# Performance work log

Measured on AMD Instinct MI355X. Metric: run time of the kernel, lower is better.

Reference implementation:

```python
import jax, jax.numpy as jnp
import numpy as np

N_NODES = 20000
N_EDGES = 320000
D_IN = 128
D_HID = 128
D_OUT = 128
HEADS = 4
NEG_SLOPE = 0.2
BN_EPS = 1e-5


def _gat_conv(x, src, dst, W, a_src, a_dst, b):
    """PyG GATConv with concat=False (mean over heads). Self-loops already in src/dst."""
    N = x.shape[0]
    H, C = a_src.shape
    h = (x @ W).reshape(N, H, C)                     # [N,H,C] per-head projections
    alpha_s = jnp.sum(h * a_src, axis=-1)            # [N,H]
    alpha_d = jnp.sum(h * a_dst, axis=-1)            # [N,H]
    logits = jax.nn.leaky_relu(alpha_s[src] + alpha_d[dst], NEG_SLOPE)  # [E,H]
    # segment softmax over incoming edges of each destination node
    m = jax.ops.segment_max(logits, dst, num_segments=N)               # [N,H]
    e = jnp.exp(logits - m[dst])
    z = jax.ops.segment_sum(e, dst, num_segments=N)                     # [N,H]
    alpha = e / (z[dst] + 1e-16)                                        # [E,H]
    msg = h[src] * alpha[:, :, None]                                    # [E,H,C]
    out = jax.ops.segment_sum(msg, dst, num_segments=N)                 # [N,H,C]
    return jnp.mean(out, axis=1) + b                                    # [N,C]


def _bn(x, gamma, beta):
    mu = jnp.mean(x, axis=0)
    var = jnp.var(x, axis=0)
    return (x - mu) * jax.lax.rsqrt(var + BN_EPS) * gamma + beta


def setup_inputs() -> dict:
    key = jax.random.key(0)
    ks = jax.random.split(key, 24)
    inp = {
        'x': jax.random.normal(ks[0], (N_NODES, D_IN), jnp.float32),
        'edge_index': jax.random.randint(ks[1], (2, N_EDGES), 0, N_NODES, jnp.int64),
        'edge_attr': jax.random.normal(ks[2], (N_EDGES, 16), jnp.float32),
    }
    def glorot(k, shape):
        fan = sum(shape) if len(shape) > 1 else shape[0]
        return jax.random.normal(k, shape, jnp.float32) * np.float32(np.sqrt(2.0 / fan))
    dims = [(D_IN, D_HID), (D_HID, D_HID), (D_HID, D_OUT)]
    for i, (din, dout) in enumerate(dims):
        inp[f'W{i}'] = glorot(ks[3 + 4 * i], (din, HEADS * dout))
        inp[f'asrc{i}'] = glorot(ks[4 + 4 * i], (HEADS, dout))
        inp[f'adst{i}'] = glorot(ks[5 + 4 * i], (HEADS, dout))
        inp[f'b{i}'] = jnp.zeros((dout,), jnp.float32)
    for i in range(2):
        inp[f'gamma{i}'] = jnp.ones((D_HID,), jnp.float32)
        inp[f'beta{i}'] = jnp.zeros((D_HID,), jnp.float32)
    return inp


def reference(x, edge_index, edge_attr, W0, asrc0, adst0, b0, gamma0, beta0,
              W1, asrc1, adst1, b1, gamma1, beta1, W2, asrc2, adst2, b2):
    N = x.shape[0]
    ar = jnp.arange(N, dtype=edge_index.dtype)
    src = jnp.concatenate([edge_index[0], ar])  # add self-loops (PyG default)
    dst = jnp.concatenate([edge_index[1], ar])
    h = _gat_conv(x, src, dst, W0, asrc0, adst0, b0)
    h = jax.nn.relu(_bn(h, gamma0, beta0))
    h = _gat_conv(h, src, dst, W1, asrc1, adst1, b1)
    h = jax.nn.relu(_bn(h, gamma1, beta1))
    out = _gat_conv(h, src, dst, W2, asrc2, adst2, b2)
    return (out, edge_attr)
```

## Files before the change

kernel.cpp:

```cpp
#include <hip/hip_runtime.h>
#include <hip/hip_fp16.h>
#include <math.h>

#define N_NODES 20000
#define N_EDGES 320000
#define EN (N_EDGES + N_NODES)
#define DIM 128
#define HEADS 4
#define DH (HEADS * DIM)
#define NEG_SLOPE 0.2f
#define BN_EPS 1e-5f

typedef _Float16 h4 __attribute__((ext_vector_type(4)));
typedef _Float16 h8 __attribute__((ext_vector_type(8)));
typedef float f4 __attribute__((ext_vector_type(4)));

__device__ __forceinline__ float lrelu(float x) { return x > 0.f ? x : NEG_SLOPE * x; }


__global__ __launch_bounds__(256) void build_edges_kernel(
    const void* __restrict__ ei_raw, int* __restrict__ src32,
    int* __restrict__ dst32, int* __restrict__ deg) {
  int e = blockIdx.x * 256 + threadIdx.x;
  if (e >= EN) return;
  const long long* ei64 = (const long long*)ei_raw;
  const int* ei32 = (const int*)ei_raw;
  bool is64 = true;
#pragma unroll
  for (int k = 0; k < 4; ++k) {
    long long v = ei64[k];
    if (v < 0 || v >= N_NODES) is64 = false;
  }
  int s, d;
  if (e < N_EDGES) {
    if (is64) { s = (int)ei64[e]; d = (int)ei64[N_EDGES + e]; }
    else      { s = ei32[e];      d = ei32[N_EDGES + e]; }
  } else {
    s = d = e - N_EDGES;
  }
  src32[e] = s;
  dst32[e] = d;
  atomicAdd(&deg[d], 1);
}

__global__ __launch_bounds__(1024) void scan_kernel(
    const int* __restrict__ deg, int* __restrict__ off) {
  __shared__ int sums[1024];
  const int tid = threadIdx.x;
  const int chunk = (N_NODES + 1023) / 1024;
  int start = tid * chunk;
  int end = start + chunk; if (end > N_NODES) end = N_NODES;
  int s = 0;
  for (int i = start; i < end && i < N_NODES; ++i) s += deg[i];
  sums[tid] = s;
  __syncthreads();
  for (int st = 1; st < 1024; st <<= 1) {
    int t = (tid >= st) ? sums[tid - st] : 0;
    __syncthreads();
    sums[tid] += t;
    __syncthreads();
  }
  int run = sums[tid] - s;
  for (int i = start; i < end && i < N_NODES; ++i) { off[i] = run; run += deg[i]; }
  if (tid == 1023) off[N_NODES] = sums[1023];
}

__global__ __launch_bounds__(256) void scatter_kernel(
    const int* __restrict__ src32, const int* __restrict__ dst32,
    const int* __restrict__ off, int* __restrict__ cursor,
    int* __restrict__ csrc) {
  int e = blockIdx.x * 256 + threadIdx.x;
  if (e >= EN) return;
  int d = dst32[e];
  int pos = atomicAdd(&cursor[d], 1);
  csrc[off[d] + pos] = src32[e];
}


__global__ __launch_bounds__(128) void wtrans_kernel(
    const float* __restrict__ W, __half* __restrict__ Wt) {
  int n = blockIdx.x;
  int k = threadIdx.x;
  Wt[(size_t)n * 128 + k] = __float2half(W[(size_t)k * 512 + n]);
}


#define SWZ(r, byte_in_row) (((r) * 256 + (byte_in_row)) ^ (((r) & 7) << 4))

__global__ __launch_bounds__(256) void gemm_mfma_kernel(
    const float* __restrict__ A, const __half* __restrict__ Wt,
    ushort* __restrict__ H16, int M) {
  __shared__ __align__(16) char Xt[64 * 256];
  __shared__ __align__(16) char Wl[64 * 256];
  int tid = threadIdx.x;
  int brow = blockIdx.x * 64;
  int bn = blockIdx.y * 64;
#pragma unroll
  for (int it = 0; it < 8; ++it) {
    int idx = it * 256 + tid;
    int r = idx >> 5, c4 = idx & 31;
    int row = brow + r;
    float4 v = make_float4(0.f, 0.f, 0.f, 0.f);
    if (row < M) v = *(const float4*)&A[(size_t)row * 128 + c4 * 4];
    h4 hv;
    hv[0] = (_Float16)v.x; hv[1] = (_Float16)v.y;
    hv[2] = (_Float16)v.z; hv[3] = (_Float16)v.w;
    *(h4*)(Xt + SWZ(r, c4 * 8)) = hv;
  }
#pragma unroll
  for (int it = 0; it < 4; ++it) {
    int idx = it * 256 + tid;
    int r = idx >> 4, c4 = idx & 15;
    uint4 v = *(const uint4*)&Wt[(size_t)(bn + r) * 128 + c4 * 8];
    *(uint4*)(Wl + SWZ(r, c4 * 16)) = v;
  }
  __syncthreads();
  int wave = tid >> 6, lane = tid & 63;
  int lrow = lane & 15, kgrp = lane >> 4;
  f4 acc[4] = {};
#pragma unroll
  for (int ks = 0; ks < 4; ++ks) {
    int kb = ks * 64 + kgrp * 16;
    int wr = wave * 16 + lrow;
    h8 af = *(h8*)(Wl + SWZ(wr, kb));
#pragma unroll
    for (int mt = 0; mt < 4; ++mt) {
      int xr = mt * 16 + lrow;
      h8 bf = *(h8*)(Xt + SWZ(xr, kb));
      acc[mt] = __builtin_amdgcn_mfma_f32_16x16x32_f16(af, bf, acc[mt], 0, 0, 0);
    }
  }
#pragma unroll
  for (int mt = 0; mt < 4; ++mt) {
    int m = brow + mt * 16 + lrow;
    if (m < M) {
      h4 hv;
#pragma unroll
      for (int i = 0; i < 4; ++i) hv[i] = (_Float16)acc[mt][i];
      *(h4*)&H16[(size_t)m * DH + bn + wave * 16 + kgrp * 4] = hv;
    }
  }
}


__global__ __launch_bounds__(256) void alpha_kernel(
    const ushort* __restrict__ H16, const float* __restrict__ a_src,
    const float* __restrict__ a_dst, float* __restrict__ as_,
    float* __restrict__ ad_) {
  int n = blockIdx.x;
  int head = threadIdx.x >> 6;
  int lane = threadIdx.x & 63;
  const __half2* hp = (const __half2*)(H16 + (size_t)n * DH) + head * 64 + lane;
  float2 h = __half22float2(*hp);
  float s = h.x * a_src[head * DIM + 2 * lane] + h.y * a_src[head * DIM + 2 * lane + 1];
  float d = h.x * a_dst[head * DIM + 2 * lane] + h.y * a_dst[head * DIM + 2 * lane + 1];
#pragma unroll
  for (int o = 32; o > 0; o >>= 1) {
    s += __shfl_xor(s, o);
    d += __shfl_xor(d, o);
  }
  if (lane == 0) {
    as_[n * 4 + head] = s;
    ad_[n * 4 + head] = d;
  }
}


__global__ __launch_bounds__(256) void smagg_kernel(
    const ushort* __restrict__ H16, const float* __restrict__ as_,
    const float* __restrict__ ad_, const int* __restrict__ off,
    const int* __restrict__ csrc, const float* __restrict__ bias,
    float* __restrict__ out, float* __restrict__ galpha) {
  __shared__ float4 alds[2][64];
  __shared__ float4 xred[2][32];
  int tid = threadIdx.x;
  int half = tid >> 7;
  int n = blockIdx.x * 2 + half;
  int wv = (tid >> 6) & 1;
  int lane = tid & 63;
  int e0 = off[n], e1 = off[n + 1];
  int deg = e1 - e0;
  bool fast = (deg <= 64);
  if (wv == 0) {
    float4 ad = *(const float4*)&ad_[n * 4];
    if (fast) {
      int i = e0 + lane;
      bool valid = lane < deg;
      float l0 = -1e30f, l1 = -1e30f, l2 = -1e30f, l3 = -1e30f;
      if (valid) {
        int s = csrc[i];
        float4 av = *(const float4*)&as_[s * 4];
        l0 = lrelu(av.x + ad.x); l1 = lrelu(av.y + ad.y);
        l2 = lrelu(av.z + ad.z); l3 = lrelu(av.w + ad.w);
      }
      float m0 = l0, m1 = l1, m2 = l2, m3 = l3;
#pragma unroll
      for (int o = 32; o > 0; o >>= 1) {
        m0 = fmaxf(m0, __shfl_xor(m0, o)); m1 = fmaxf(m1, __shfl_xor(m1, o));
        m2 = fmaxf(m2, __shfl_xor(m2, o)); m3 = fmaxf(m3, __shfl_xor(m3, o));
      }
      float p0 = valid ? expf(l0 - m0) : 0.f;
      float p1 = valid ? expf(l1 - m1) : 0.f;
      float p2 = valid ? expf(l2 - m2) : 0.f;
      float p3 = valid ? expf(l3 - m3) : 0.f;
      float z0 = p0, z1 = p1, z2 = p2, z3 = p3;
#pragma unroll
      for (int o = 32; o > 0; o >>= 1) {
        z0 += __shfl_xor(z0, o); z1 += __shfl_xor(z1, o);
        z2 += __shfl_xor(z2, o); z3 += __shfl_xor(z3, o);
      }
      if (valid) {
        alds[half][lane] = make_float4(p0 / (z0 + 1e-16f), p1 / (z1 + 1e-16f),
                                       p2 / (z2 + 1e-16f), p3 / (z3 + 1e-16f));
      }
    } else {
      float m0 = -1e30f, m1 = -1e30f, m2 = -1e30f, m3 = -1e30f;
      for (int i = e0 + lane; i < e1; i += 64) {
        int s = csrc[i];
        float4 av = *(const float4*)&as_[s * 4];
        float l0 = lrelu(av.x + ad.x), l1 = lrelu(av.y + ad.y);
        float l2 = lrelu(av.z + ad.z), l3 = lrelu(av.w + ad.w);
        ((float4*)galpha)[i] = make_float4(l0, l1, l2, l3);
        m0 = fmaxf(m0, l0); m1 = fmaxf(m1, l1);
        m2 = fmaxf(m2, l2); m3 = fmaxf(m3, l3);
      }
#pragma unroll
      for (int o = 32; o > 0; o >>= 1) {
        m0 = fmaxf(m0, __shfl_xor(m0, o)); m1 = fmaxf(m1, __shfl_xor(m1, o));
        m2 = fmaxf(m2, __shfl_xor(m2, o)); m3 = fmaxf(m3, __shfl_xor(m3, o));
      }
      float z0 = 0.f, z1 = 0.f, z2 = 0.f, z3 = 0.f;
      for (int i = e0 + lane; i < e1; i += 64) {
        float4 l = ((const float4*)galpha)[i];
        float p0 = expf(l.x - m0), p1 = expf(l.y - m1);
        float p2 = expf(l.z - m2), p3 = expf(l.w - m3);
        ((float4*)galpha)[i] = make_float4(p0, p1, p2, p3);
        z0 += p0; z1 += p1; z2 += p2; z3 += p3;
      }
#pragma unroll
      for (int o = 32; o > 0; o >>= 1) {
        z0 += __shfl_xor(z0, o); z1 += __shfl_xor(z1, o);
        z2 += __shfl_xor(z2, o); z3 += __shfl_xor(z3, o);
      }
      float r0 = 1.f / (z0 + 1e-16f), r1 = 1.f / (z1 + 1e-16f);
      float r2 = 1.f / (z2 + 1e-16f), r3 = 1.f / (z3 + 1e-16f);
      for (int i = e0 + lane; i < e1; i += 64) {
        float4 p = ((const float4*)galpha)[i];
        ((float4*)galpha)[i] = make_float4(p.x * r0, p.y * r1, p.z * r2, p.w * r3);
      }
    }
  }
  __syncthreads();
  const uint2* Hp = (const uint2*)H16;
  const float* alds_f = (const float*)&alds[half][0];
  int hh = wv * 2 + (lane >> 5);
  float a0 = 0.f, a1 = 0.f, a2 = 0.f, a3 = 0.f;
  int i = e0;
#define AGG_BODY(ii)                                                          \
  {                                                                           \
    int s = csrc[ii];                                                         \
    float w = fast ? alds_f[((ii) - e0) * 4 + hh] : galpha[(size_t)(ii) * 4 + hh]; \
    uint2 hvv = Hp[(size_t)s * 128 + wv * 64 + lane];                         \
    float2 lo = __half22float2(*(__half2*)&hvv.x);                            \
    float2 hi = __half22float2(*(__half2*)&hvv.y);                            \
    a0 += w * lo.x; a1 += w * lo.y; a2 += w * hi.x; a3 += w * hi.y;           \
  }
  for (; i + 3 < e1; i += 4) { AGG_BODY(i) AGG_BODY(i + 1) AGG_BODY(i + 2) AGG_BODY(i + 3) }
  for (; i < e1; ++i) AGG_BODY(i)
#undef AGG_BODY
  a0 += __shfl_xor(a0, 32); a1 += __shfl_xor(a1, 32);
  a2 += __shfl_xor(a2, 32); a3 += __shfl_xor(a3, 32);
  if (wv == 1 && lane < 32) xred[half][lane] = make_float4(a0, a1, a2, a3);
  __syncthreads();
  if (wv == 0 && lane < 32) {
    float4 o2 = xred[half][lane];
    float4 bv = *(const float4*)&bias[lane * 4];
    float4 r;
    r.x = 0.25f * (a0 + o2.x) + bv.x;
    r.y = 0.25f * (a1 + o2.y) + bv.y;
    r.z = 0.25f * (a2 + o2.z) + bv.z;
    r.w = 0.25f * (a3 + o2.w) + bv.w;
    *(float4*)&out[(size_t)n * DIM + lane * 4] = r;
  }
}


__global__ __launch_bounds__(256) void bn_stats_kernel(
    const float* __restrict__ X, float* __restrict__ stats) {
  int c = threadIdx.x & 127;
  int half = threadIdx.x >> 7;
  float s = 0.f, s2 = 0.f;
  for (int r = blockIdx.x * 2 + half; r < N_NODES; r += gridDim.x * 2) {
    float v = X[(size_t)r * DIM + c];
    s += v;
    s2 += v * v;
  }
  atomicAdd(&stats[c], s);
  atomicAdd(&stats[DIM + c], s2);
}

__global__ __launch_bounds__(256) void bn_apply_kernel(
    float* __restrict__ X, const float* __restrict__ stats,
    const float* __restrict__ gamma, const float* __restrict__ beta) {
  int idx = blockIdx.x * 256 + threadIdx.x;
  if (idx >= N_NODES * DIM) return;
  int c = idx & 127;
  const float invN = 1.f / (float)N_NODES;
  float mean = stats[c] * invN;
  float var = stats[DIM + c] * invN - mean * mean;
  float scale = gamma[c] * rsqrtf(var + BN_EPS);
  float shift = beta[c] - mean * scale;
  float v = X[idx] * scale + shift;
  X[idx] = fmaxf(v, 0.f);
}


extern "C" void kernel_launch(void* const* d_in, const int* in_sizes, int n_in,
                              void* d_out, int out_size, void* d_ws, size_t ws_size,
                              hipStream_t stream) {
  (void)in_sizes; (void)n_in; (void)out_size; (void)ws_size;
  const float* x = (const float*)d_in[0];
  const void* ei = d_in[1];
  const float* eattr = (const float*)d_in[2];
  const float* W[3]    = {(const float*)d_in[3],  (const float*)d_in[7],  (const float*)d_in[11]};
  const float* asrc[3] = {(const float*)d_in[4],  (const float*)d_in[8],  (const float*)d_in[12]};
  const float* adst[3] = {(const float*)d_in[5],  (const float*)d_in[9],  (const float*)d_in[13]};
  const float* bias[3] = {(const float*)d_in[6],  (const float*)d_in[10], (const float*)d_in[14]};
  const float* gamma[2] = {(const float*)d_in[15], (const float*)d_in[17]};
  const float* beta[2]  = {(const float*)d_in[16], (const float*)d_in[18]};

  char* ws = (char*)d_ws;
  size_t o = 0;
  auto alloc = [&](size_t bytes) -> void* {
    void* p = ws + o;
    o += (bytes + 255) & ~(size_t)255;
    return p;
  };
  int* deg      = (int*)alloc(N_NODES * 4);
  int* cursor   = (int*)alloc(N_NODES * 4);
  float* stats0 = (float*)alloc(2 * DIM * 4);
  float* stats1 = (float*)alloc(2 * DIM * 4);
  size_t zero_bytes = o;
  int* off    = (int*)alloc((N_NODES + 1) * 4);
  int* src32  = (int*)alloc((size_t)EN * 4);
  int* dst32  = (int*)alloc((size_t)EN * 4);
  int* csrc   = (int*)alloc((size_t)EN * 4);
  float* galpha = (float*)alloc((size_t)EN * 4 * 4);
  ushort* H16  = (ushort*)alloc((size_t)N_NODES * DH * 2);
  float* Ob    = (float*)alloc((size_t)N_NODES * DIM * 4);
  float* as_   = (float*)alloc((size_t)N_NODES * 4 * 4);
  float* ad_   = (float*)alloc((size_t)N_NODES * 4 * 4);
  __half* Wt[3];
  for (int L = 0; L < 3; ++L) Wt[L] = (__half*)alloc((size_t)DH * 128 * 2);

  hipMemsetAsync(d_ws, 0, zero_bytes, stream);

  build_edges_kernel<<<(EN + 255) / 256, 256, 0, stream>>>(ei, src32, dst32, deg);
  scan_kernel<<<1, 1024, 0, stream>>>(deg, off);
  scatter_kernel<<<(EN + 255) / 256, 256, 0, stream>>>(src32, dst32, off, cursor, csrc);
  for (int L = 0; L < 3; ++L)
    wtrans_kernel<<<DH, 128, 0, stream>>>(W[L], Wt[L]);

  const float* in_ptr = x;
  for (int L = 0; L < 3; ++L) {
    gemm_mfma_kernel<<<dim3((N_NODES + 63) / 64, DH / 64), 256, 0, stream>>>(
        in_ptr, Wt[L], H16, N_NODES);
    alpha_kernel<<<N_NODES, 256, 0, stream>>>(H16, asrc[L], adst[L], as_, ad_);
    float* outp = (L == 2) ? (float*)d_out : Ob;
    smagg_kernel<<<N_NODES / 2, 256, 0, stream>>>(H16, as_, ad_, off, csrc,
                                                  bias[L], outp, galpha);
    if (L < 2) {
      float* st = (L == 0) ? stats0 : stats1;
      bn_stats_kernel<<<256, 256, 0, stream>>>(Ob, st);
      bn_apply_kernel<<<(N_NODES * DIM + 255) / 256, 256, 0, stream>>>(
          Ob, st, gamma[L], beta[L]);
      in_ptr = Ob;
    }
  }

  hipMemcpyAsync((float*)d_out + (size_t)N_NODES * DIM, eattr,
                 (size_t)N_EDGES * 16 * 4, hipMemcpyDeviceToDevice, stream);
}
```

Measured before the change: 536.4 us.

## Fuse alpha and BN-apply into GEMM, widen aggregation to one wave per node

The GEMM kernel now computes the per-head attention dot products from its accumulators, which removes the separate alpha kernel and its re-read of H16. It also applies the BatchNorm scale/shift and ReLU while loading its input, so a small coefficient kernel replaces the full bn_apply pass. The aggregation kernel maps one wave per node with 16-byte gathers and an 8-way unroll, dropping the LDS cross-wave reduction and __syncthreads. The three weight transposes are merged into one launch. Each GEMM block now loops over four N-chunks, which cuts the grid width and adds serial work per block.

```diff
diff --git a/kernel.cpp b/kernel.cpp
--- a/kernel.cpp
+++ b/kernel.cpp
@@ -78,90 +78,143 @@
 
 
 __global__ __launch_bounds__(128) void wtrans_kernel(
-    const float* __restrict__ W, __half* __restrict__ Wt) {
+    const float* __restrict__ W0, const float* __restrict__ W1,
+    const float* __restrict__ W2, __half* __restrict__ T0,
+    __half* __restrict__ T1, __half* __restrict__ T2) {
   int n = blockIdx.x;
   int k = threadIdx.x;
-  Wt[(size_t)n * 128 + k] = __float2half(W[(size_t)k * 512 + n]);
+  const float* W = (blockIdx.y == 0) ? W0 : (blockIdx.y == 1) ? W1 : W2;
+  __half* T = (blockIdx.y == 0) ? T0 : (blockIdx.y == 1) ? T1 : T2;
+  T[(size_t)n * 128 + k] = __float2half(W[(size_t)k * 512 + n]);
+}
+
+
+__global__ __launch_bounds__(128) void bn_coef_kernel(
+    const float* __restrict__ stats, const float* __restrict__ gamma,
+    const float* __restrict__ beta, float* __restrict__ coef) {
+  int c = threadIdx.x;
+  const float invN = 1.f / (float)N_NODES;
+  float mean = stats[c] * invN;
+  float var = stats[DIM + c] * invN - mean * mean;
+  float scale = gamma[c] * rsqrtf(var + BN_EPS);
+  coef[c] = scale;
+  coef[DIM + c] = beta[c] - mean * scale;
 }
 
 
 #define SWZ(r, byte_in_row) (((r) * 256 + (byte_in_row)) ^ (((r) & 7) << 4))
 
-__global__ __launch_bounds__(256) void gemm_mfma_kernel(
+__global__ __launch_bounds__(256) void gemm_fused_kernel(
     const float* __restrict__ A, const __half* __restrict__ Wt,
-    ushort* __restrict__ H16, int M) {
+    const float* __restrict__ coef, int apply_bn,
+    const float* __restrict__ a_src, const float* __restrict__ a_dst,
+    ushort* __restrict__ H16, float* __restrict__ as_,
+    float* __restrict__ ad_, int M) {
   __shared__ __align__(16) char Xt[64 * 256];
   __shared__ __align__(16) char Wl[64 * 256];
+  __shared__ float red_as[4][4][2][16];
+  __shared__ float red_ad[4][4][2][16];
   int tid = threadIdx.x;
   int brow = blockIdx.x * 64;
-  int bn = blockIdx.y * 64;
+  int half_id = blockIdx.y;
+  const float4* coef4 = (const float4*)coef;
 #pragma unroll
   for (int it = 0; it < 8; ++it) {
     int idx = it * 256 + tid;
     int r = idx >> 5, c4 = idx & 31;
     int row = brow + r;
     float4 v = make_float4(0.f, 0.f, 0.f, 0.f);
-    if (row < M) v = *(const float4*)&A[(size_t)row * 128 + c4 * 4];
+    if (row < M) {
+      v = *(const float4*)&A[(size_t)row * 128 + c4 * 4];
+      if (apply_bn) {
+        float4 sc = coef4[c4], sh = coef4[32 + c4];
+        v.x = fmaxf(v.x * sc.x + sh.x, 0.f);
+        v.y = fmaxf(v.y * sc.y + sh.y, 0.f);
+        v.z = fmaxf(v.z * sc.z + sh.z, 0.f);
+        v.w = fmaxf(v.w * sc.w + sh.w, 0.f);
+      }
+    }
     h4 hv;
     hv[0] = (_Float16)v.x; hv[1] = (_Float16)v.y;
     hv[2] = (_Float16)v.z; hv[3] = (_Float16)v.w;
     *(h4*)(Xt + SWZ(r, c4 * 8)) = hv;
   }
-#pragma unroll
-  for (int it = 0; it < 4; ++it) {
-    int idx = it * 256 + tid;
-    int r = idx >> 4, c4 = idx & 15;
-    uint4 v = *(const uint4*)&Wt[(size_t)(bn + r) * 128 + c4 * 8];
-    *(uint4*)(Wl + SWZ(r, c4 * 16)) = v;
-  }
-  __syncthreads();
   int wave = tid >> 6, lane = tid & 63;
   int lrow = lane & 15, kgrp = lane >> 4;
-  f4 acc[4] = {};
-#pragma unroll
-  for (int ks = 0; ks < 4; ++ks) {
-    int kb = ks * 64 + kgrp * 16;
-    int wr = wave * 16 + lrow;
-    h8 af = *(h8*)(Wl + SWZ(wr, kb));
+  float asum[4][2] = {}, adsum[4][2] = {};
+  for (int nc = 0; nc < 4; ++nc) {
+    int chunk = half_id * 4 + nc;
+    int hh = nc >> 1;
+    __syncthreads();
+#pragma unroll
+    for (int it = 0; it < 4; ++it) {
+      int idx = it * 256 + tid;
+      int r = idx >> 4, c4 = idx & 15;
+      uint4 v = *(const uint4*)&Wt[(size_t)(chunk * 64 + r) * 128 + c4 * 8];
+      *(uint4*)(Wl + SWZ(r, c4 * 16)) = v;
+    }
+    __syncthreads();
+    f4 acc[4] = {};
+#pragma unroll
+    for (int ks = 0; ks < 4; ++ks) {
+      int kb = ks * 64 + kgrp * 16;
+      h8 af = *(h8*)(Wl + SWZ(wave * 16 + lrow, kb));
+#pragma unroll
+      for (int mt = 0; mt < 4; ++mt) {
+        h8 bf = *(h8*)(Xt + SWZ(mt * 16 + lrow, kb));
+        acc[mt] = __builtin_amdgcn_mfma_f32_16x16x32_f16(af, bf, acc[mt], 0, 0, 0);
+      }
+    }
+    int n_base = chunk * 64 + wave * 16 + kgrp * 4;
+    float4 as4 = *(const float4*)&a_src[n_base];
+    float4 ad4 = *(const float4*)&a_dst[n_base];
 #pragma unroll
     for (int mt = 0; mt < 4; ++mt) {
-      int xr = mt * 16 + lrow;
-      h8 bf = *(h8*)(Xt + SWZ(xr, kb));
-      acc[mt] = __builtin_amdgcn_mfma_f32_16x16x32_f16(af, bf, acc[mt], 0, 0, 0);
-    }
-  }
-#pragma unroll
-  for (int mt = 0; mt < 4; ++mt) {
-    int m = brow + mt * 16 + lrow;
+      int m = brow + mt * 16 + lrow;
+      if (m < M) {
+        h4 hv;
+#pragma unroll
+        for (int i = 0; i < 4; ++i) hv[i] = (_Float16)acc[mt][i];
+        *(h4*)&H16[(size_t)m * DH + n_base] = hv;
+      }
+      asum[mt][hh] += acc[mt][0] * as4.x + acc[mt][1] * as4.y +
+                      acc[mt][2] * as4.z + acc[mt][3] * as4.w;
+      adsum[mt][hh] += acc[mt][0] * ad4.x + acc[mt][1] * ad4.y +
+                       acc[mt][2] * ad4.z + acc[mt][3] * ad4.w;
+    }
+  }
+#pragma unroll
+  for (int mt = 0; mt < 4; ++mt)
+#pragma unroll
+    for (int hh = 0; hh < 2; ++hh) {
+      asum[mt][hh] += __shfl_xor(asum[mt][hh], 16);
+      asum[mt][hh] += __shfl_xor(asum[mt][hh], 32);
+      adsum[mt][hh] += __shfl_xor(adsum[mt][hh], 16);
+      adsum[mt][hh] += __shfl_xor(adsum[mt][hh], 32);
+    }
+  __syncthreads();
+  if (lane < 16) {
+#pragma unroll
+    for (int mt = 0; mt < 4; ++mt)
+#pragma unroll
+      for (int hh = 0; hh < 2; ++hh) {
+        red_as[wave][mt][hh][lrow] = asum[mt][hh];
+        red_ad[wave][mt][hh][lrow] = adsum[mt][hh];
+      }
+  }
+  __syncthreads();
+  if (tid < 128) {
+    int mt = tid >> 5, hh = (tid >> 4) & 1, lr = tid & 15;
+    float s = red_as[0][mt][hh][lr] + red_as[1][mt][hh][lr] +
+              red_as[2][mt][hh][lr] + red_as[3][mt][hh][lr];
+    float d = red_ad[0][mt][hh][lr] + red_ad[1][mt][hh][lr] +
+              red_ad[2][mt][hh][lr] + red_ad[3][mt][hh][lr];
+    int m = brow + mt * 16 + lr;
     if (m < M) {
-      h4 hv;
-#pragma unroll
-      for (int i = 0; i < 4; ++i) hv[i] = (_Float16)acc[mt][i];
-      *(h4*)&H16[(size_t)m * DH + bn + wave * 16 + kgrp * 4] = hv;
-    }
-  }
-}
-
-
-__global__ __launch_bounds__(256) void alpha_kernel(
-    const ushort* __restrict__ H16, const float* __restrict__ a_src,
-    const float* __restrict__ a_dst, float* __restrict__ as_,
-    float* __restrict__ ad_) {
-  int n = blockIdx.x;
-  int head = threadIdx.x >> 6;
-  int lane = threadIdx.x & 63;
-  const __half2* hp = (const __half2*)(H16 + (size_t)n * DH) + head * 64 + lane;
-  float2 h = __half22float2(*hp);
-  float s = h.x * a_src[head * DIM + 2 * lane] + h.y * a_src[head * DIM + 2 * lane + 1];
-  float d = h.x * a_dst[head * DIM + 2 * lane] + h.y * a_dst[head * DIM + 2 * lane + 1];
-#pragma unroll
-  for (int o = 32; o > 0; o >>= 1) {
-    s += __shfl_xor(s, o);
-    d += __shfl_xor(d, o);
-  }
-  if (lane == 0) {
-    as_[n * 4 + head] = s;
-    ad_[n * 4 + head] = d;
+      int head = half_id * 2 + hh;
+      as_[m * 4 + head] = s;
+      ad_[m * 4 + head] = d;
+    }
   }
 }
 
@@ -171,116 +224,122 @@
     const float* __restrict__ ad_, const int* __restrict__ off,
     const int* __restrict__ csrc, const float* __restrict__ bias,
     float* __restrict__ out, float* __restrict__ galpha) {
-  __shared__ float4 alds[2][64];
-  __shared__ float4 xred[2][32];
+  __shared__ float alds[4][64 * 4];
   int tid = threadIdx.x;
-  int half = tid >> 7;
-  int n = blockIdx.x * 2 + half;
-  int wv = (tid >> 6) & 1;
+  int slot = tid >> 6;
+  int n = blockIdx.x * 4 + slot;
   int lane = tid & 63;
   int e0 = off[n], e1 = off[n + 1];
   int deg = e1 - e0;
   bool fast = (deg <= 64);
-  if (wv == 0) {
-    float4 ad = *(const float4*)&ad_[n * 4];
-    if (fast) {
-      int i = e0 + lane;
-      bool valid = lane < deg;
-      float l0 = -1e30f, l1 = -1e30f, l2 = -1e30f, l3 = -1e30f;
-      if (valid) {
-        int s = csrc[i];
-        float4 av = *(const float4*)&as_[s * 4];
-        l0 = lrelu(av.x + ad.x); l1 = lrelu(av.y + ad.y);
-        l2 = lrelu(av.z + ad.z); l3 = lrelu(av.w + ad.w);
-      }
-      float m0 = l0, m1 = l1, m2 = l2, m3 = l3;
-#pragma unroll
-      for (int o = 32; o > 0; o >>= 1) {
-        m0 = fmaxf(m0, __shfl_xor(m0, o)); m1 = fmaxf(m1, __shfl_xor(m1, o));
-        m2 = fmaxf(m2, __shfl_xor(m2, o)); m3 = fmaxf(m3, __shfl_xor(m3, o));
-      }
-      float p0 = valid ? expf(l0 - m0) : 0.f;
-      float p1 = valid ? expf(l1 - m1) : 0.f;
-      float p2 = valid ? expf(l2 - m2) : 0.f;
-      float p3 = valid ? expf(l3 - m3) : 0.f;
-      float z0 = p0, z1 = p1, z2 = p2, z3 = p3;
-#pragma unroll
-      for (int o = 32; o > 0; o >>= 1) {
-        z0 += __shfl_xor(z0, o); z1 += __shfl_xor(z1, o);
-        z2 += __shfl_xor(z2, o); z3 += __shfl_xor(z3, o);
-      }
-      if (valid) {
-        alds[half][lane] = make_float4(p0 / (z0 + 1e-16f), p1 / (z1 + 1e-16f),
-                                       p2 / (z2 + 1e-16f), p3 / (z3 + 1e-16f));
-      }
-    } else {
-      float m0 = -1e30f, m1 = -1e30f, m2 = -1e30f, m3 = -1e30f;
-      for (int i = e0 + lane; i < e1; i += 64) {
-        int s = csrc[i];
-        float4 av = *(const float4*)&as_[s * 4];
-        float l0 = lrelu(av.x + ad.x), l1 = lrelu(av.y + ad.y);
-        float l2 = lrelu(av.z + ad.z), l3 = lrelu(av.w + ad.w);
-        ((float4*)galpha)[i] = make_float4(l0, l1, l2, l3);
-        m0 = fmaxf(m0, l0); m1 = fmaxf(m1, l1);
-        m2 = fmaxf(m2, l2); m3 = fmaxf(m3, l3);
-      }
-#pragma unroll
-      for (int o = 32; o > 0; o >>= 1) {
-        m0 = fmaxf(m0, __shfl_xor(m0, o)); m1 = fmaxf(m1, __shfl_xor(m1, o));
-        m2 = fmaxf(m2, __shfl_xor(m2, o)); m3 = fmaxf(m3, __shfl_xor(m3, o));
-      }
-      float z0 = 0.f, z1 = 0.f, z2 = 0.f, z3 = 0.f;
-      for (int i = e0 + lane; i < e1; i += 64) {
-        float4 l = ((const float4*)galpha)[i];
-        float p0 = expf(l.x - m0), p1 = expf(l.y - m1);
-        float p2 = expf(l.z - m2), p3 = expf(l.w - m3);
-        ((float4*)galpha)[i] = make_float4(p0, p1, p2, p3);
-        z0 += p0; z1 += p1; z2 += p2; z3 += p3;
-      }
-#pragma unroll
-      for (int o = 32; o > 0; o >>= 1) {
-        z0 += __shfl_xor(z0, o); z1 += __shfl_xor(z1, o);
-        z2 += __shfl_xor(z2, o); z3 += __shfl_xor(z3, o);
-      }
-      float r0 = 1.f / (z0 + 1e-16f), r1 = 1.f / (z1 + 1e-16f);
-      float r2 = 1.f / (z2 + 1e-16f), r3 = 1.f / (z3 + 1e-16f);
-      for (int i = e0 + lane; i < e1; i += 64) {
-        float4 p = ((const float4*)galpha)[i];
-        ((float4*)galpha)[i] = make_float4(p.x * r0, p.y * r1, p.z * r2, p.w * r3);
-      }
-    }
-  }
-  __syncthreads();
-  const uint2* Hp = (const uint2*)H16;
-  const float* alds_f = (const float*)&alds[half][0];
-  int hh = wv * 2 + (lane >> 5);
-  float a0 = 0.f, a1 = 0.f, a2 = 0.f, a3 = 0.f;
+  float4 ad = *(const float4*)&ad_[n * 4];
+  if (fast) {
+    bool valid = lane < deg;
+    float l0 = -1e30f, l1 = -1e30f, l2 = -1e30f, l3 = -1e30f;
+    if (valid) {
+      int s = csrc[e0 + lane];
+      float4 av = *(const float4*)&as_[s * 4];
+      l0 = lrelu(av.x + ad.x); l1 = lrelu(av.y + ad.y);
+      l2 = lrelu(av.z + ad.z); l3 = lrelu(av.w + ad.w);
+    }
+    float m0 = l0, m1 = l1, m2 = l2, m3 = l3;
+#pragma unroll
+    for (int o = 32; o > 0; o >>= 1) {
+      m0 = fmaxf(m0, __shfl_xor(m0, o)); m1 = fmaxf(m1, __shfl_xor(m1, o));
+      m2 = fmaxf(m2, __shfl_xor(m2, o)); m3 = fmaxf(m3, __shfl_xor(m3, o));
+    }
+    float p0 = valid ? expf(l0 - m0) : 0.f;
+    float p1 = valid ? expf(l1 - m1) : 0.f;
+    float p2 = valid ? expf(l2 - m2) : 0.f;
+    float p3 = valid ? expf(l3 - m3) : 0.f;
+    float z0 = p0, z1 = p1, z2 = p2, z3 = p3;
+#pragma unroll
+    for (int o = 32; o > 0; o >>= 1) {
+      z0 += __shfl_xor(z0, o); z1 += __shfl_xor(z1, o);
+      z2 += __shfl_xor(z2, o); z3 += __shfl_xor(z3, o);
+    }
+    if (valid) {
+      float4 r = make_float4(p0 / (z0 + 1e-16f), p1 / (z1 + 1e-16f),
+                             p2 / (z2 + 1e-16f), p3 / (z3 + 1e-16f));
+      *(float4*)&alds[slot][lane * 4] = r;
+    }
+  } else {
+    float m0 = -1e30f, m1 = -1e30f, m2 = -1e30f, m3 = -1e30f;
+    for (int i = e0 + lane; i < e1; i += 64) {
+      int s = csrc[i];
+      float4 av = *(const float4*)&as_[s * 4];
+      float l0 = lrelu(av.x + ad.x), l1 = lrelu(av.y + ad.y);
+      float l2 = lrelu(av.z + ad.z), l3 = lrelu(av.w + ad.w);
+      ((float4*)galpha)[i] = make_float4(l0, l1, l2, l3);
+      m0 = fmaxf(m0, l0); m1 = fmaxf(m1, l1);
+      m2 = fmaxf(m2, l2); m3 = fmaxf(m3, l3);
+    }
+#pragma unroll
+    for (int o = 32; o > 0; o >>= 1) {
+      m0 = fmaxf(m0, __shfl_xor(m0, o)); m1 = fmaxf(m1, __shfl_xor(m1, o));
+      m2 = fmaxf(m2, __shfl_xor(m2, o)); m3 = fmaxf(m3, __shfl_xor(m3, o));
+    }
+    float z0 = 0.f, z1 = 0.f, z2 = 0.f, z3 = 0.f;
+    for (int i = e0 + lane; i < e1; i += 64) {
+      float4 l = ((const float4*)galpha)[i];
+      float p0 = expf(l.x - m0), p1 = expf(l.y - m1);
+      float p2 = expf(l.z - m2), p3 = expf(l.w - m3);
+      ((float4*)galpha)[i] = make_float4(p0, p1, p2, p3);
+      z0 += p0; z1 += p1; z2 += p2; z3 += p3;
+    }
+#pragma unroll
+    for (int o = 32; o > 0; o >>= 1) {
+      z0 += __shfl_xor(z0, o); z1 += __shfl_xor(z1, o);
+      z2 += __shfl_xor(z2, o); z3 += __shfl_xor(z3, o);
+    }
+    float r0 = 1.f / (z0 + 1e-16f), r1 = 1.f / (z1 + 1e-16f);
+    float r2 = 1.f / (z2 + 1e-16f), r3 = 1.f / (z3 + 1e-16f);
+    for (int i = e0 + lane; i < e1; i += 64) {
+      float4 p = ((const float4*)galpha)[i];
+      ((float4*)galpha)[i] = make_float4(p.x * r0, p.y * r1, p.z * r2, p.w * r3);
+    }
+  }
+  const uint4* Hp = (const uint4*)H16;
+  const float* af = &alds[slot][0];
+  int head = lane >> 4;
+  float acc[8] = {};
+#define AGG_BODY(ii)                                                       \
+  {                                                                        \
+    int s = csrc[ii];                                                      \
+    float w = fast ? af[((ii) - e0) * 4 + head]                            \
+                   : galpha[(size_t)(ii) * 4 + head];                      \
+    uint4 hv = Hp[(size_t)s * 64 + lane];                                  \
+    float2 f0 = __half22float2(*(__half2*)&hv.x);                          \
+    float2 f1 = __half22float2(*(__half2*)&hv.y);                          \
+    float2 f2 = __half22float2(*(__half2*)&hv.z);                          \
+    float2 f3 = __half22float2(*(__half2*)&hv.w);                          \
+    acc[0] += w * f0.x; acc[1] += w * f0.y;                                \
+    acc[2] += w * f1.x; acc[3] += w * f1.y;                                \
+    acc[4] += w * f2.x; acc[5] += w * f2.y;                                \
+    acc[6] += w * f3.x; acc[7] += w * f3.y;                                \
+  }
   int i = e0;
-#define AGG_BODY(ii)                                                          \
-  {                                                                           \
-    int s = csrc[ii];                                                         \
-    float w = fast ? alds_f[((ii) - e0) * 4 + hh] : galpha[(size_t)(ii) * 4 + hh]; \
-    uint2 hvv = Hp[(size_t)s * 128 + wv * 64 + lane];                         \
-    float2 lo = __half22float2(*(__half2*)&hvv.x);                            \
-    float2 hi = __half22float2(*(__half2*)&hvv.y);                            \
-    a0 += w * lo.x; a1 += w * lo.y; a2 += w * hi.x; a3 += w * hi.y;           \
-  }
-  for (; i + 3 < e1; i += 4) { AGG_BODY(i) AGG_BODY(i + 1) AGG_BODY(i + 2) AGG_BODY(i + 3) }
+  for (; i + 7 < e1; i += 8) {
+    AGG_BODY(i)     AGG_BODY(i + 1) AGG_BODY(i + 2) AGG_BODY(i + 3)
+    AGG_BODY(i + 4) AGG_BODY(i + 5) AGG_BODY(i + 6) AGG_BODY(i + 7)
+  }
   for (; i < e1; ++i) AGG_BODY(i)
 #undef AGG_BODY
-  a0 += __shfl_xor(a0, 32); a1 += __shfl_xor(a1, 32);
-  a2 += __shfl_xor(a2, 32); a3 += __shfl_xor(a3, 32);
-  if (wv == 1 && lane < 32) xred[half][lane] = make_float4(a0, a1, a2, a3);
-  __syncthreads();
-  if (wv == 0 && lane < 32) {
-    float4 o2 = xred[half][lane];
-    float4 bv = *(const float4*)&bias[lane * 4];
-    float4 r;
-    r.x = 0.25f * (a0 + o2.x) + bv.x;
-    r.y = 0.25f * (a1 + o2.y) + bv.y;
-    r.z = 0.25f * (a2 + o2.z) + bv.z;
-    r.w = 0.25f * (a3 + o2.w) + bv.w;
-    *(float4*)&out[(size_t)n * DIM + lane * 4] = r;
+#pragma unroll
+  for (int j = 0; j < 8; ++j) {
+    acc[j] += __shfl_xor(acc[j], 16);
+    acc[j] += __shfl_xor(acc[j], 32);
+  }
+  if (lane < 16) {
+    int c0 = lane * 8;
+    float4 b0 = *(const float4*)&bias[c0];
+    float4 b1 = *(const float4*)&bias[c0 + 4];
+    float4 r0 = make_float4(0.25f * acc[0] + b0.x, 0.25f * acc[1] + b0.y,
+                            0.25f * acc[2] + b0.z, 0.25f * acc[3] + b0.w);
+    float4 r1 = make_float4(0.25f * acc[4] + b1.x, 0.25f * acc[5] + b1.y,
+                            0.25f * acc[6] + b1.z, 0.25f * acc[7] + b1.w);
+    *(float4*)&out[(size_t)n * DIM + c0] = r0;
+    *(float4*)&out[(size_t)n * DIM + c0 + 4] = r1;
   }
 }
 
@@ -288,30 +347,15 @@
 __global__ __launch_bounds__(256) void bn_stats_kernel(
     const float* __restrict__ X, float* __restrict__ stats) {
   int c = threadIdx.x & 127;
-  int half = threadIdx.x >> 7;
+  int hlf = threadIdx.x >> 7;
   float s = 0.f, s2 = 0.f;
-  for (int r = blockIdx.x * 2 + half; r < N_NODES; r += gridDim.x * 2) {
+  for (int r = blockIdx.x * 2 + hlf; r < N_NODES; r += gridDim.x * 2) {
     float v = X[(size_t)r * DIM + c];
     s += v;
     s2 += v * v;
   }
   atomicAdd(&stats[c], s);
   atomicAdd(&stats[DIM + c], s2);
-}
-
-__global__ __launch_bounds__(256) void bn_apply_kernel(
-    float* __restrict__ X, const float* __restrict__ stats,
-    const float* __restrict__ gamma, const float* __restrict__ beta) {
-  int idx = blockIdx.x * 256 + threadIdx.x;
-  if (idx >= N_NODES * DIM) return;
-  int c = idx & 127;
-  const float invN = 1.f / (float)N_NODES;
-  float mean = stats[c] * invN;
-  float var = stats[DIM + c] * invN - mean * mean;
-  float scale = gamma[c] * rsqrtf(var + BN_EPS);
-  float shift = beta[c] - mean * scale;
-  float v = X[idx] * scale + shift;
-  X[idx] = fmaxf(v, 0.f);
 }
 
 
@@ -350,6 +394,8 @@
   float* Ob    = (float*)alloc((size_t)N_NODES * DIM * 4);
   float* as_   = (float*)alloc((size_t)N_NODES * 4 * 4);
   float* ad_   = (float*)alloc((size_t)N_NODES * 4 * 4);
+  float* coef0 = (float*)alloc(2 * DIM * 4);
+  float* coef1 = (float*)alloc(2 * DIM * 4);
   __half* Wt[3];
   for (int L = 0; L < 3; ++L) Wt[L] = (__half*)alloc((size_t)DH * 128 * 2);
 
@@ -358,22 +404,22 @@
   build_edges_kernel<<<(EN + 255) / 256, 256, 0, stream>>>(ei, src32, dst32, deg);
   scan_kernel<<<1, 1024, 0, stream>>>(deg, off);
   scatter_kernel<<<(EN + 255) / 256, 256, 0, stream>>>(src32, dst32, off, cursor, csrc);
-  for (int L = 0; L < 3; ++L)
-    wtrans_kernel<<<DH, 128, 0, stream>>>(W[L], Wt[L]);
+  wtrans_kernel<<<dim3(DH, 3), 128, 0, stream>>>(W[0], W[1], W[2], Wt[0], Wt[1], Wt[2]);
 
   const float* in_ptr = x;
+  const float* coefs[3] = {coef0, coef0, coef1};
   for (int L = 0; L < 3; ++L) {
-    gemm_mfma_kernel<<<dim3((N_NODES + 63) / 64, DH / 64), 256, 0, stream>>>(
-        in_ptr, Wt[L], H16, N_NODES);
-    alpha_kernel<<<N_NODES, 256, 0, stream>>>(H16, asrc[L], adst[L], as_, ad_);
+    gemm_fused_kernel<<<dim3((N_NODES + 63) / 64, 2), 256, 0, stream>>>(
+        in_ptr, Wt[L], coefs[L], (L > 0) ? 1 : 0, asrc[L], adst[L],
+        H16, as_, ad_, N_NODES);
     float* outp = (L == 2) ? (float*)d_out : Ob;
-    smagg_kernel<<<N_NODES / 2, 256, 0, stream>>>(H16, as_, ad_, off, csrc,
+    smagg_kernel<<<N_NODES / 4, 256, 0, stream>>>(H16, as_, ad_, off, csrc,
                                                   bias[L], outp, galpha);
     if (L < 2) {
       float* st = (L == 0) ? stats0 : stats1;
+      float* cf = (L == 0) ? coef0 : coef1;
       bn_stats_kernel<<<256, 256, 0, stream>>>(Ob, st);
-      bn_apply_kernel<<<(N_NODES * DIM + 255) / 256, 256, 0, stream>>>(
-          Ob, st, gamma[L], beta[L]);
+      bn_coef_kernel<<<1, 128, 0, stream>>>(st, gamma[L], beta[L], cf);
       in_ptr = Ob;
     }
   }
```

Measured after the change: 444.6 us. 17.1% less time.
